# Performance work log

Hardware: AMD Instinct MI355X
Metric: run time of the kernel (lower is better)

## Reference

```python
import jax, jax.numpy as jnp
import numpy as np

N_NODES = 50000
N_EDGES = 800000
D_FEAT = 128
D_HID = 128
N_CLASSES = 16


def setup_inputs() -> dict:
    key = jax.random.key(0)
    ks = jax.random.split(key, 5)
    x = jax.random.normal(ks[0], (N_NODES, D_FEAT), dtype=jnp.float32)
    edge_index = jax.random.randint(ks[1], (2, N_EDGES), 0, N_NODES, dtype=jnp.int32)
    # Glorot-ish scaled weights to keep activations in a sane range
    W1 = jax.random.normal(ks[2], (D_FEAT, D_HID), dtype=jnp.float32) * 0.05
    b1 = jnp.zeros((D_HID,), dtype=jnp.float32)
    W2 = jax.random.normal(ks[3], (D_HID, N_CLASSES), dtype=jnp.float32) * 0.05
    b2 = jnp.zeros((N_CLASSES,), dtype=jnp.float32)
    return {"x": x, "edge_index": edge_index, "W1": W1, "b1": b1, "W2": W2, "b2": b2}


def _gcn_conv(h, src, dst, norm, W, b, num_nodes):
    # linear transform first (F_in >= F_out ordering as in PyG GCNConv)
    h = h @ W                              # [N, F_out]
    msg = h[src] * norm[:, None]           # gather + edge-wise scale  [E+N, F_out]
    out = jax.ops.segment_sum(msg, dst, num_segments=num_nodes)  # scatter-add
    return out + b


def reference(x, edge_index, W1, b1, W2, b2):
    n = x.shape[0]
    loop = jnp.arange(n, dtype=edge_index.dtype)
    src = jnp.concatenate([edge_index[0], loop])  # add self-loops
    dst = jnp.concatenate([edge_index[1], loop])
    # symmetric normalization: deg^{-1/2}[src] * deg^{-1/2}[dst]
    deg = jax.ops.segment_sum(jnp.ones_like(dst, dtype=x.dtype), dst, num_segments=n)
    dis = jax.lax.rsqrt(jnp.maximum(deg, 1.0))  # deg >= 1 thanks to self-loops
    norm = dis[src] * dis[dst]
    h = jax.nn.relu(_gcn_conv(x, src, dst, norm, W1, b1, n))
    # dropout is identity in eval mode
    out = _gcn_conv(h, src, dst, norm, W2, b2, n)
    return jax.nn.sigmoid(out)
```

## Files before the change

### kernel.cpp

```cpp
#include <hip/hip_runtime.h>
#include <math.h>

#define NN 50000
#define NE 800000
#define DF 128
#define NC 16
#define WLD 136
#define NBIN 391
#define EPB 8192
#define HB ((NE + EPB - 1) / EPB)
#define HL (NBIN * HB)
#define PB ((HL + 255) / 256)
#define GB ((NN + 63) / 64)

typedef __bf16 bf16x8 __attribute__((ext_vector_type(8)));
typedef __bf16 bf16x4 __attribute__((ext_vector_type(4)));
typedef __bf16 bf16x2 __attribute__((ext_vector_type(2)));
typedef float  f32x4  __attribute__((ext_vector_type(4)));
typedef float  f32x2  __attribute__((ext_vector_type(2)));

__global__ __launch_bounds__(256) void k_hist(const int* __restrict__ dst,
                                              int* __restrict__ h) {
    __shared__ int hc[NBIN];
    const int bb = blockIdx.x, t = threadIdx.x;
    for (int i = t; i < NBIN; i += 256) hc[i] = 0;
    __syncthreads();
    const int base = bb * EPB;
#pragma unroll
    for (int i = 0; i < EPB / 256; ++i) {
        int e = base + i * 256 + t;
        if (e < NE) atomicAdd(&hc[dst[e] >> 7], 1);
    }
    __syncthreads();
    for (int i = t; i < NBIN; i += 256) h[i * HB + bb] = hc[i];
}

__global__ __launch_bounds__(256) void k_hpart(const int* __restrict__ h,
                                               int* __restrict__ part) {
    __shared__ int ws[4];
    const int b = blockIdx.x, t = threadIdx.x;
    const int idx = b * 256 + t;
    int s = (idx < HL) ? h[idx] : 0;
    for (int o = 32; o > 0; o >>= 1) s += __shfl_down(s, o);
    if ((t & 63) == 0) ws[t >> 6] = s;
    __syncthreads();
    if (t == 0) part[b] = ws[0] + ws[1] + ws[2] + ws[3];
}

__global__ __launch_bounds__(256) void k_hscan_part(const int* __restrict__ part,
                                                    int* __restrict__ partoff,
                                                    int* __restrict__ hscan,
                                                    const float* __restrict__ W2,
                                                    __bf16* __restrict__ W2T) {
    __shared__ int s[256];
    const int t = threadIdx.x;
    for (int i = t; i < NC * DF; i += 256) {
        int n = i >> 7, k = i & 127;
        W2T[i] = (__bf16)W2[k * NC + n];
    }
    int v = (t < PB) ? part[t] : 0;
    s[t] = v;
    __syncthreads();
    for (int o = 1; o < 256; o <<= 1) {
        int x = (t >= o) ? s[t - o] : 0;
        __syncthreads();
        s[t] += x;
        __syncthreads();
    }
    if (t < PB) partoff[t] = s[t] - v;
    if (t == 255) hscan[HL] = s[255];
}

__global__ __launch_bounds__(256) void k_hoff(const int* __restrict__ h,
                                              const int* __restrict__ partoff,
                                              int* __restrict__ hscan) {
    __shared__ int s[256];
    const int b = blockIdx.x, t = threadIdx.x;
    const int idx = b * 256 + t;
    int v = (idx < HL) ? h[idx] : 0;
    s[t] = v;
    __syncthreads();
    for (int o = 1; o < 256; o <<= 1) {
        int x = (t >= o) ? s[t - o] : 0;
        __syncthreads();
        s[t] += x;
        __syncthreads();
    }
    if (idx < HL) hscan[idx] = partoff[b] + s[t] - v;
}

__global__ __launch_bounds__(256) void k_gemm1_scatter(const float* __restrict__ X,
                                                       const float* __restrict__ W1,
                                                       unsigned char* __restrict__ H1,
                                                       const int* __restrict__ src,
                                                       const int* __restrict__ dst,
                                                       const int* __restrict__ hscan,
                                                       int* __restrict__ ebuf) {
    __shared__ __bf16 wlds[DF * WLD];
    __shared__ int cur[NBIN];
    if (blockIdx.x >= GB) {
        const int bb = blockIdx.x - GB;
        const int t = threadIdx.x;
        for (int i = t; i < NBIN; i += 256) cur[i] = hscan[i * HB + bb];
        __syncthreads();
        const int base = bb * EPB;
#pragma unroll
        for (int i = 0; i < EPB / 256; ++i) {
            int e = base + i * 256 + t;
            if (e < NE) {
                int s = src[e], d = dst[e];
                int pos = atomicAdd(&cur[d >> 7], 1);
                ebuf[pos] = s | ((d & 127) << 16);
            }
        }
        return;
    }
    const int wid = threadIdx.x >> 6, lane = threadIdx.x & 63;
    const int m0 = blockIdx.x * 64 + wid * 16;
    const int m = m0 + (lane & 15);
    const int mc = (m < NN) ? m : NN - 1;
    const int l15 = lane & 15;
    const int kb = (lane >> 4) * 8;

    float4 xf[8];
#pragma unroll
    for (int q = 0; q < 4; ++q) {
        xf[2 * q]     = *(const float4*)&X[(size_t)mc * DF + q * 32 + kb];
        xf[2 * q + 1] = *(const float4*)&X[(size_t)mc * DF + q * 32 + kb + 4];
    }
    for (int i = threadIdx.x; i < DF * DF; i += 256) {
        int k = i >> 7, n = i & 127;
        wlds[n * WLD + k] = (__bf16)W1[i];
    }
    __syncthreads();

    f32x4 acc[8];
#pragma unroll
    for (int nf = 0; nf < 8; ++nf) acc[nf] = (f32x4){0.f, 0.f, 0.f, 0.f};
#pragma unroll
    for (int ks = 0; ks < 4; ++ks) {
        float4 x0 = xf[2 * ks], x1 = xf[2 * ks + 1];
        bf16x8 xa;
        xa[0] = (__bf16)x0.x; xa[1] = (__bf16)x0.y; xa[2] = (__bf16)x0.z; xa[3] = (__bf16)x0.w;
        xa[4] = (__bf16)x1.x; xa[5] = (__bf16)x1.y; xa[6] = (__bf16)x1.z; xa[7] = (__bf16)x1.w;
#pragma unroll
        for (int nf = 0; nf < 8; ++nf) {
            bf16x8 wa = *(const bf16x8*)&wlds[(nf * 16 + l15) * WLD + ks * 32 + kb];
            acc[nf] = __builtin_amdgcn_mfma_f32_16x16x32_bf16(wa, xa, acc[nf], 0, 0, 0);
        }
    }
    if (m < NN) {
#pragma unroll
        for (int nf = 0; nf < 8; ++nf) {
            int pw = __builtin_amdgcn_cvt_pk_fp8_f32(acc[nf][0], acc[nf][1], 0, false);
            pw = __builtin_amdgcn_cvt_pk_fp8_f32(acc[nf][2], acc[nf][3], pw, true);
            *(unsigned int*)&H1[(size_t)m * DF + nf * 16 + (lane >> 4) * 4] = (unsigned int)pw;
        }
    }
}

__global__ __launch_bounds__(256) void k_rankB(const int* __restrict__ ebuf,
                                               const int* __restrict__ hscan,
                                               int* __restrict__ off,
                                               float* __restrict__ dis,
                                               unsigned short* __restrict__ rec) {
    __shared__ int cnt[128], s[256], cur[128];
    const int bin = blockIdx.x, t = threadIdx.x;
    const int base = hscan[bin * HB];
    const int end  = hscan[(bin + 1) * HB];
    if (t < 128) cnt[t] = 0;
    __syncthreads();
    for (int e = base + t; e < end; e += 256)
        atomicAdd(&cnt[(ebuf[e] >> 16) & 127], 1);
    __syncthreads();
    int c = (t < 128) ? cnt[t] : 0;
    s[t] = c;
    __syncthreads();
    for (int o = 1; o < 256; o <<= 1) {
        int x = (t >= o) ? s[t - o] : 0;
        __syncthreads();
        s[t] += x;
        __syncthreads();
    }
    int lo = s[t] - c;
    int d = (bin << 7) + t;
    if (t < 128 && d < NN) {
        off[d] = base + lo;
        dis[d] = rsqrtf((float)(c + 1));
    }
    if (bin == NBIN - 1 && t == 0) off[NN] = NE;
    if (t < 128) cur[t] = base + lo;
    __syncthreads();
    for (int e = base + t; e < end; e += 256) {
        int ed = ebuf[e];
        int p = atomicAdd(&cur[(ed >> 16) & 127], 1);
        rec[p] = (unsigned short)(ed & 0xFFFF);
    }
}

__global__ __launch_bounds__(256) void k_agg1g2(const unsigned char* __restrict__ H1,
                                                const float* __restrict__ dis,
                                                const float* __restrict__ b1,
                                                const __bf16* __restrict__ W2T,
                                                const int* __restrict__ off,
                                                const unsigned short* __restrict__ rec,
                                                __bf16* __restrict__ H2) {
    const int wid = threadIdx.x >> 6, lane = threadIdx.x & 63;
    const int n = blockIdx.x * 4 + wid;
    if (n >= NN) return;
    const int g = lane >> 4, l16 = lane & 15;
    const int fo = l16 * 8;
    const float dn = dis[n];

    float a[8];
#pragma unroll
    for (int i = 0; i < 8; ++i) a[i] = 0.f;

    const int e0 = off[n], e1 = off[n + 1];
    int e = e0 + g;
    for (; e + 12 < e1; e += 16) {
        int r0 = rec[e];
        int r1 = rec[e + 4];
        int r2 = rec[e + 8];
        int r3 = rec[e + 12];
        float w0 = dis[r0], w1 = dis[r1], w2 = dis[r2], w3 = dis[r3];
        uint2 u0 = *(const uint2*)&H1[(size_t)r0 * DF + fo];
        uint2 u1 = *(const uint2*)&H1[(size_t)r1 * DF + fo];
        uint2 u2 = *(const uint2*)&H1[(size_t)r2 * DF + fo];
        uint2 u3 = *(const uint2*)&H1[(size_t)r3 * DF + fo];
#define ACC8(u, w)                                                        \
        {                                                                 \
            f32x2 p0 = __builtin_amdgcn_cvt_pk_f32_fp8((u).x, false);     \
            f32x2 p1 = __builtin_amdgcn_cvt_pk_f32_fp8((u).x, true);      \
            f32x2 p2 = __builtin_amdgcn_cvt_pk_f32_fp8((u).y, false);     \
            f32x2 p3 = __builtin_amdgcn_cvt_pk_f32_fp8((u).y, true);      \
            a[0] += p0[0] * (w); a[1] += p0[1] * (w);                     \
            a[2] += p1[0] * (w); a[3] += p1[1] * (w);                     \
            a[4] += p2[0] * (w); a[5] += p2[1] * (w);                     \
            a[6] += p3[0] * (w); a[7] += p3[1] * (w);                     \
        }
        ACC8(u0, w0) ACC8(u1, w1) ACC8(u2, w2) ACC8(u3, w3)
    }
    for (; e < e1; e += 4) {
        int r = rec[e];
        float w = dis[r];
        uint2 u = *(const uint2*)&H1[(size_t)r * DF + fo];
        ACC8(u, w)
    }
#undef ACC8
#pragma unroll
    for (int i = 0; i < 8; ++i) {
        a[i] += __shfl_xor(a[i], 16);
        a[i] += __shfl_xor(a[i], 32);
    }
    {
        const float d2 = dn * dn;
        float4 b0 = *(const float4*)&b1[fo];
        float4 b4 = *(const float4*)&b1[fo + 4];
        uint2 us = *(const uint2*)&H1[(size_t)n * DF + fo];
        f32x2 s0 = __builtin_amdgcn_cvt_pk_f32_fp8(us.x, false);
        f32x2 s1 = __builtin_amdgcn_cvt_pk_f32_fp8(us.x, true);
        f32x2 s2 = __builtin_amdgcn_cvt_pk_f32_fp8(us.y, false);
        f32x2 s3 = __builtin_amdgcn_cvt_pk_f32_fp8(us.y, true);
        a[0] = fmaxf(a[0] * dn + s0[0] * d2 + b0.x, 0.f);
        a[1] = fmaxf(a[1] * dn + s0[1] * d2 + b0.y, 0.f);
        a[2] = fmaxf(a[2] * dn + s1[0] * d2 + b0.z, 0.f);
        a[3] = fmaxf(a[3] * dn + s1[1] * d2 + b0.w, 0.f);
        a[4] = fmaxf(a[4] * dn + s2[0] * d2 + b4.x, 0.f);
        a[5] = fmaxf(a[5] * dn + s2[1] * d2 + b4.y, 0.f);
        a[6] = fmaxf(a[6] * dn + s3[0] * d2 + b4.z, 0.f);
        a[7] = fmaxf(a[7] * dn + s3[1] * d2 + b4.w, 0.f);
    }

    float p[4];
#pragma unroll
    for (int j = 0; j < 4; ++j) {
        bf16x8 wr = *(const bf16x8*)&W2T[(size_t)(g * 4 + j) * DF + fo];
        float s = 0.f;
#pragma unroll
        for (int i = 0; i < 8; ++i) s += a[i] * (float)wr[i];
        p[j] = s;
    }
#pragma unroll
    for (int o = 1; o <= 8; o <<= 1) {
#pragma unroll
        for (int j = 0; j < 4; ++j) p[j] += __shfl_xor(p[j], o);
    }
    if (l16 == 0) {
        bf16x4 o4;
        o4[0] = (__bf16)p[0]; o4[1] = (__bf16)p[1];
        o4[2] = (__bf16)p[2]; o4[3] = (__bf16)p[3];
        *(bf16x4*)&H2[(size_t)n * NC + g * 4] = o4;
    }
}

__global__ __launch_bounds__(256) void k_agg2(const __bf16* __restrict__ H2,
                                              const float* __restrict__ dis,
                                              const float* __restrict__ b2,
                                              const int* __restrict__ off,
                                              const unsigned short* __restrict__ rec,
                                              float* __restrict__ OUT) {
    const int wid = threadIdx.x >> 6, lane = threadIdx.x & 63;
    const int n = blockIdx.x * 4 + wid;
    if (n >= NN) return;
    const float dn = dis[n];

    const int g = lane >> 3, l8 = lane & 7;
    float ax = 0.f, ay = 0.f;
    const int e0 = off[n], e1 = off[n + 1];
    int e = e0 + g;
    for (; e + 8 < e1; e += 16) {
        int r0 = rec[e];
        int r1 = rec[e + 8];
        float w0 = dis[r0], w1 = dis[r1];
        bf16x2 h0 = *(const bf16x2*)&H2[(size_t)r0 * NC + l8 * 2];
        bf16x2 h1 = *(const bf16x2*)&H2[(size_t)r1 * NC + l8 * 2];
        ax += (float)h0[0] * w0;
        ay += (float)h0[1] * w0;
        ax += (float)h1[0] * w1;
        ay += (float)h1[1] * w1;
    }
    for (; e < e1; e += 8) {
        int r = rec[e];
        float w = dis[r];
        bf16x2 h = *(const bf16x2*)&H2[(size_t)r * NC + l8 * 2];
        ax += (float)h[0] * w;
        ay += (float)h[1] * w;
    }
    ax += __shfl_xor(ax, 8);  ay += __shfl_xor(ay, 8);
    ax += __shfl_xor(ax, 16); ay += __shfl_xor(ay, 16);
    ax += __shfl_xor(ax, 32); ay += __shfl_xor(ay, 32);
    if (g == 0) {
        float d2 = dn * dn;
        bf16x2 hs = *(const bf16x2*)&H2[(size_t)n * NC + l8 * 2];
        float2 bb = *(const float2*)&b2[l8 * 2];
        float vx = ax * dn + (float)hs[0] * d2 + bb.x;
        float vy = ay * dn + (float)hs[1] * d2 + bb.y;
        float2 o = { 1.0f / (1.0f + expf(-vx)), 1.0f / (1.0f + expf(-vy)) };
        *(float2*)&OUT[(size_t)n * NC + l8 * 2] = o;
    }
}

extern "C" void kernel_launch(void* const* d_in, const int* in_sizes, int n_in,
                              void* d_out, int out_size, void* d_ws, size_t ws_size,
                              hipStream_t stream) {
    const float* X  = (const float*)d_in[0];
    const int*   EI = (const int*)d_in[1];
    const float* W1 = (const float*)d_in[2];
    const float* b1 = (const float*)d_in[3];
    const float* W2 = (const float*)d_in[4];
    const float* b2 = (const float*)d_in[5];
    float* OUT = (float*)d_out;

    const int* src = EI;
    const int* dst = EI + NE;

    char* ws = (char*)d_ws;
    int*    h       = (int*)(ws);
    int*    hscan   = (int*)(ws + 163840);
    int*    hpart   = (int*)(ws + 327680);
    int*    hpartoff= (int*)(ws + 331776);
    int*    off     = (int*)(ws + 335872);
    float*  dis     = (float*)(ws + 540672);
    __bf16* W2T     = (__bf16*)(ws + 745472);
    int*    ebuf    = (int*)(ws + 749568);
    unsigned short* rec = (unsigned short*)(ws + 3949568);
    unsigned char* H1 = (unsigned char*)(ws + 5549568);
    __bf16* H2      = (__bf16*)(ws + 11949568);

    const int B = 256;

    k_hist<<<HB, B, 0, stream>>>(dst, h);
    k_hpart<<<PB, B, 0, stream>>>(h, hpart);
    k_hscan_part<<<1, B, 0, stream>>>(hpart, hpartoff, hscan, W2, W2T);
    k_hoff<<<PB, B, 0, stream>>>(h, hpartoff, hscan);
    k_gemm1_scatter<<<GB + HB, B, 0, stream>>>(X, W1, H1, src, dst, hscan, ebuf);
    k_rankB<<<NBIN, B, 0, stream>>>(ebuf, hscan, off, dis, rec);

    k_agg1g2<<<(NN + 3) / 4, B, 0, stream>>>(H1, dis, b1, W2T, off, rec, H2);
    k_agg2<<<(NN + 3) / 4, B, 0, stream>>>(H2, dis, b2, off, rec, OUT);
}
```

Baseline: 104.5 us.

## Replace per-block histogram scan with global bin totals and atomic cursor reservation

The per-block bin histogram and its three-kernel hierarchical scan are replaced by global atomic bin totals, a single 512-thread scan over 391 bins, and per-block atomic reservation of output ranges in the scatter kernel. This cuts two kernel launches and the large histogram matrix traffic. In exchange it adds a memset, a second dst histogram pass inside the scatter blocks, and global atomics. Edge order within a bin becomes nondeterministic, but k_rankB re-sorts by destination, so only the order of summation changes.

```diff
diff --git a/kernel.cpp b/kernel.cpp
--- a/kernel.cpp
+++ b/kernel.cpp
@@ -9,8 +9,6 @@
 #define NBIN 391
 #define EPB 8192
 #define HB ((NE + EPB - 1) / EPB)
-#define HL (NBIN * HB)
-#define PB ((HL + 255) / 256)
 #define GB ((NN + 63) / 64)
 
 typedef __bf16 bf16x8 __attribute__((ext_vector_type(8)));
@@ -20,7 +18,7 @@
 typedef float  f32x2  __attribute__((ext_vector_type(2)));
 
 __global__ __launch_bounds__(256) void k_hist(const int* __restrict__ dst,
-                                              int* __restrict__ h) {
+                                              int* __restrict__ gtot) {
     __shared__ int hc[NBIN];
     const int bb = blockIdx.x, t = threadIdx.x;
     for (int i = t; i < NBIN; i += 256) hc[i] = 0;
@@ -32,61 +30,36 @@
         if (e < NE) atomicAdd(&hc[dst[e] >> 7], 1);
     }
     __syncthreads();
-    for (int i = t; i < NBIN; i += 256) h[i * HB + bb] = hc[i];
-}
-
-__global__ __launch_bounds__(256) void k_hpart(const int* __restrict__ h,
-                                               int* __restrict__ part) {
-    __shared__ int ws[4];
-    const int b = blockIdx.x, t = threadIdx.x;
-    const int idx = b * 256 + t;
-    int s = (idx < HL) ? h[idx] : 0;
-    for (int o = 32; o > 0; o >>= 1) s += __shfl_down(s, o);
-    if ((t & 63) == 0) ws[t >> 6] = s;
-    __syncthreads();
-    if (t == 0) part[b] = ws[0] + ws[1] + ws[2] + ws[3];
-}
-
-__global__ __launch_bounds__(256) void k_hscan_part(const int* __restrict__ part,
-                                                    int* __restrict__ partoff,
-                                                    int* __restrict__ hscan,
-                                                    const float* __restrict__ W2,
-                                                    __bf16* __restrict__ W2T) {
-    __shared__ int s[256];
+    for (int i = t; i < NBIN; i += 256)
+        if (hc[i]) atomicAdd(&gtot[i], hc[i]);
+}
+
+__global__ __launch_bounds__(512) void k_binscan(const int* __restrict__ gtot,
+                                                 int* __restrict__ binscan,
+                                                 int* __restrict__ gcur,
+                                                 const float* __restrict__ W2,
+                                                 __bf16* __restrict__ W2T) {
+    __shared__ int s[512];
     const int t = threadIdx.x;
-    for (int i = t; i < NC * DF; i += 256) {
+    for (int i = t; i < NC * DF; i += 512) {
         int n = i >> 7, k = i & 127;
         W2T[i] = (__bf16)W2[k * NC + n];
     }
-    int v = (t < PB) ? part[t] : 0;
+    int v = (t < NBIN) ? gtot[t] : 0;
     s[t] = v;
     __syncthreads();
-    for (int o = 1; o < 256; o <<= 1) {
+    for (int o = 1; o < 512; o <<= 1) {
         int x = (t >= o) ? s[t - o] : 0;
         __syncthreads();
         s[t] += x;
         __syncthreads();
     }
-    if (t < PB) partoff[t] = s[t] - v;
-    if (t == 255) hscan[HL] = s[255];
-}
-
-__global__ __launch_bounds__(256) void k_hoff(const int* __restrict__ h,
-                                              const int* __restrict__ partoff,
-                                              int* __restrict__ hscan) {
-    __shared__ int s[256];
-    const int b = blockIdx.x, t = threadIdx.x;
-    const int idx = b * 256 + t;
-    int v = (idx < HL) ? h[idx] : 0;
-    s[t] = v;
-    __syncthreads();
-    for (int o = 1; o < 256; o <<= 1) {
-        int x = (t >= o) ? s[t - o] : 0;
-        __syncthreads();
-        s[t] += x;
-        __syncthreads();
-    }
-    if (idx < HL) hscan[idx] = partoff[b] + s[t] - v;
+    if (t < NBIN) {
+        int base = s[t] - v;
+        binscan[t] = base;
+        gcur[t] = base;
+    }
+    if (t == 511) binscan[NBIN] = NE;
 }
 
 __global__ __launch_bounds__(256) void k_gemm1_scatter(const float* __restrict__ X,
@@ -94,16 +67,25 @@
                                                        unsigned char* __restrict__ H1,
                                                        const int* __restrict__ src,
                                                        const int* __restrict__ dst,
-                                                       const int* __restrict__ hscan,
+                                                       int* __restrict__ gcur,
                                                        int* __restrict__ ebuf) {
     __shared__ __bf16 wlds[DF * WLD];
-    __shared__ int cur[NBIN];
+    __shared__ int hc[NBIN], cur[NBIN];
     if (blockIdx.x >= GB) {
         const int bb = blockIdx.x - GB;
         const int t = threadIdx.x;
-        for (int i = t; i < NBIN; i += 256) cur[i] = hscan[i * HB + bb];
+        for (int i = t; i < NBIN; i += 256) hc[i] = 0;
         __syncthreads();
         const int base = bb * EPB;
+#pragma unroll
+        for (int i = 0; i < EPB / 256; ++i) {
+            int e = base + i * 256 + t;
+            if (e < NE) atomicAdd(&hc[dst[e] >> 7], 1);
+        }
+        __syncthreads();
+        for (int i = t; i < NBIN; i += 256)
+            cur[i] = hc[i] ? atomicAdd(&gcur[i], hc[i]) : 0;
+        __syncthreads();
 #pragma unroll
         for (int i = 0; i < EPB / 256; ++i) {
             int e = base + i * 256 + t;
@@ -160,14 +142,14 @@
 }
 
 __global__ __launch_bounds__(256) void k_rankB(const int* __restrict__ ebuf,
-                                               const int* __restrict__ hscan,
+                                               const int* __restrict__ binscan,
                                                int* __restrict__ off,
                                                float* __restrict__ dis,
                                                unsigned short* __restrict__ rec) {
     __shared__ int cnt[128], s[256], cur[128];
     const int bin = blockIdx.x, t = threadIdx.x;
-    const int base = hscan[bin * HB];
-    const int end  = hscan[(bin + 1) * HB];
+    const int base = binscan[bin];
+    const int end  = binscan[bin + 1];
     if (t < 128) cnt[t] = 0;
     __syncthreads();
     for (int e = base + t; e < end; e += 256)
@@ -356,27 +338,24 @@
     const int* dst = EI + NE;
 
     char* ws = (char*)d_ws;
-    int*    h       = (int*)(ws);
-    int*    hscan   = (int*)(ws + 163840);
-    int*    hpart   = (int*)(ws + 327680);
-    int*    hpartoff= (int*)(ws + 331776);
-    int*    off     = (int*)(ws + 335872);
-    float*  dis     = (float*)(ws + 540672);
-    __bf16* W2T     = (__bf16*)(ws + 745472);
-    int*    ebuf    = (int*)(ws + 749568);
-    unsigned short* rec = (unsigned short*)(ws + 3949568);
-    unsigned char* H1 = (unsigned char*)(ws + 5549568);
-    __bf16* H2      = (__bf16*)(ws + 11949568);
+    int*    gtot    = (int*)(ws);
+    int*    binscan = (int*)(ws + 4096);
+    int*    gcur    = (int*)(ws + 8192);
+    int*    off     = (int*)(ws + 12288);
+    float*  dis     = (float*)(ws + 217088);
+    __bf16* W2T     = (__bf16*)(ws + 421888);
+    int*    ebuf    = (int*)(ws + 425984);
+    unsigned short* rec = (unsigned short*)(ws + 3625984);
+    unsigned char* H1 = (unsigned char*)(ws + 5225984);
+    __bf16* H2      = (__bf16*)(ws + 11625984);
 
     const int B = 256;
 
-    k_hist<<<HB, B, 0, stream>>>(dst, h);
-    k_hpart<<<PB, B, 0, stream>>>(h, hpart);
-    k_hscan_part<<<1, B, 0, stream>>>(hpart, hpartoff, hscan, W2, W2T);
-    k_hoff<<<PB, B, 0, stream>>>(h, hpartoff, hscan);
-    k_gemm1_scatter<<<GB + HB, B, 0, stream>>>(X, W1, H1, src, dst, hscan, ebuf);
-    k_rankB<<<NBIN, B, 0, stream>>>(ebuf, hscan, off, dis, rec);
-
+    hipMemsetAsync(gtot, 0, NBIN * sizeof(int), stream);
+    k_hist<<<HB, B, 0, stream>>>(dst, gtot);
+    k_binscan<<<1, 512, 0, stream>>>(gtot, binscan, gcur, W2, W2T);
+    k_gemm1_scatter<<<GB + HB, B, 0, stream>>>(X, W1, H1, src, dst, gcur, ebuf);
+    k_rankB<<<NBIN, B, 0, stream>>>(ebuf, binscan, off, dis, rec);
     k_agg1g2<<<(NN + 3) / 4, B, 0, stream>>>(H1, dis, b1, W2T, off, rec, H2);
     k_agg2<<<(NN + 3) / 4, B, 0, stream>>>(H2, dis, b2, off, rec, OUT);
 }
```

Result: slower. 113.4 us (+8.5%).
